# Optimization experiments

Hardware: AMD Instinct MI355X
Metric: run time of the kernel (lower is better)

## Reference

```python
import jax, jax.numpy as jnp
import numpy as np

B, H, S, D = 4, 16, 2048, 64  # head_dim = num_dims // num_heads = 1024 // 16


def setup_inputs() -> dict:
    key = jax.random.key(0)
    kq, kk, kv = jax.random.split(key, 3)
    q = jax.random.normal(kq, (B, H, S, D), dtype=jnp.float32)
    k = jax.random.normal(kk, (B, H, S, D), dtype=jnp.float32)
    v = jax.random.normal(kv, (B, H, S, D), dtype=jnp.float32)
    return {"q": q, "k": k, "v": v}


def reference(q, k, v):
    # scores = (q @ k^T) / sqrt(head_dim)  -> [B, H, S, S]
    scale = 1.0 / np.sqrt(D).astype(np.float32)
    scores = jnp.einsum("bhqd,bhkd->bhqk", q, k) * scale
    # softmax over keys; dropout rate is 0.0 (eval), so it's the identity
    weights = jax.nn.softmax(scores, axis=-1)
    # weights @ v -> [B, H, S, D]
    return jnp.einsum("bhqk,bhkd->bhqd", weights, v)
```

## Files before the change

### kernel.cpp

```cpp
#include <hip/hip_runtime.h>
#include <hip/hip_bf16.h>

#define S_LEN 2048
#define BH_TOTAL 64
#define D_DIM 64
#define NT 32

typedef float f32x4 __attribute__((ext_vector_type(4)));
typedef __bf16 bf16x8 __attribute__((ext_vector_type(8)));
typedef unsigned short u16x8 __attribute__((ext_vector_type(8)));
typedef unsigned int u32;
typedef u32 u32x2 __attribute__((ext_vector_type(2)));

union BF8 { u16x8 u; bf16x8 b; };

#if __has_builtin(__builtin_amdgcn_exp2f)
#define EX2(x) __builtin_amdgcn_exp2f(x)
#else
#define EX2(x) exp2f(x)
#endif

__device__ __forceinline__ unsigned short f2b(float f) {
  __bf16 h = (__bf16)f;
  return __builtin_bit_cast(unsigned short, h);
}
__device__ __forceinline__ u32 pk2(float a, float b) {
  return (u32)f2b(a) | ((u32)f2b(b) << 16);
}

__device__ __forceinline__ void gload16(const unsigned short* g, unsigned short* l) {
  __builtin_amdgcn_global_load_lds(
      (const __attribute__((address_space(1))) unsigned int*)g,
      (__attribute__((address_space(3))) unsigned int*)l, 16, 0, 0);
}

__global__ __launch_bounds__(256)
void cvt_k(const float* __restrict__ K, unsigned short* __restrict__ Kb) {
  int i = blockIdx.x * 256 + threadIdx.x;
  const f32x4* src = (const f32x4*)K;
  f32x4 a = src[2 * i], b = src[2 * i + 1];
  u16x8 o;
  #pragma unroll
  for (int j = 0; j < 4; ++j) { o[j] = f2b(a[j]); o[j + 4] = f2b(b[j]); }
  ((u16x8*)Kb)[i] = o;
}

__global__ __launch_bounds__(256)
void tr_v(const float* __restrict__ V, unsigned short* __restrict__ Vt) {
  __shared__ unsigned short T[64][72];
  int bh = blockIdx.x >> 5, t5 = blockIdx.x & 31;
  int s0 = t5 * 64;
  int tid = threadIdx.x;
  {
    int s = tid >> 2, d0 = (tid & 3) * 16;
    const float* src = V + ((size_t)bh * S_LEN + s0 + s) * D_DIM + d0;
    #pragma unroll
    for (int j = 0; j < 16; j += 4) {
      f32x4 x = *(const f32x4*)(src + j);
      #pragma unroll
      for (int q2 = 0; q2 < 4; ++q2) T[d0 + j + q2][s] = f2b(x[q2]);
    }
  }
  __syncthreads();
  {
    int d = tid >> 2, c0 = (tid & 3) * 16;
    unsigned short* dst = Vt + ((size_t)bh * D_DIM + d) * S_LEN + s0 + c0;
    u16x8 o;
    #pragma unroll
    for (int q2 = 0; q2 < 8; ++q2) o[q2] = T[d][c0 + q2];
    *(u16x8*)dst = o;
    #pragma unroll
    for (int q2 = 0; q2 < 8; ++q2) o[q2] = T[d][c0 + 8 + q2];
    *(u16x8*)(dst + 8) = o;
  }
}

__global__ __launch_bounds__(512, 4)
void attn_fwd(const float* __restrict__ Q, const unsigned short* __restrict__ Kb,
              const unsigned short* __restrict__ Vt, float* __restrict__ O) {
  const int wg = blockIdx.x;
  const int id = (wg & 7) * 64 + (wg >> 3);
  const int qt = id & 7;
  const int bh = id >> 3;

  const int tid = threadIdx.x;
  const int w = tid >> 6;
  const int ln = tid & 63;
  const int lr = ln & 15;
  const int lg = ln >> 4;

  __shared__ __align__(16) unsigned short Ks[2][4096];
  __shared__ __align__(16) unsigned short Vs[2][4096];
  __shared__ __align__(16) unsigned short Ps[8][2048];

  const size_t hbase = (size_t)bh * S_LEN * D_DIM;
  const unsigned short* Kh = Kb + hbase;
  const unsigned short* Vh = Vt + hbase;

  const int q0 = qt * 256 + w * 32;
  BF8 qf[2][2];
  {
    const float sc = 0.125f * 1.44269504088896f;
    #pragma unroll
    for (int qg = 0; qg < 2; ++qg) {
      const float* qp = Q + hbase + (size_t)(q0 + qg * 16 + lr) * D_DIM + lg * 8;
      #pragma unroll
      for (int f = 0; f < 2; ++f) {
        f32x4 a = *(const f32x4*)(qp + f * 32);
        f32x4 b = *(const f32x4*)(qp + f * 32 + 4);
        #pragma unroll
        for (int j = 0; j < 4; ++j) {
          qf[qg][f].u[j]     = f2b(a[j] * sc);
          qf[qg][f].u[j + 4] = f2b(b[j] * sc);
        }
      }
    }
  }

  const int srow = ln >> 3;
  const int scol = ((ln & 7) ^ srow) * 8;
  const unsigned short* ks0 = Kh + (size_t)(w * 8 + srow) * D_DIM + scol;
  const unsigned short* vs0 = Vh + (size_t)(w * 8 + srow) * S_LEN + scol;

  const int swz = (lr & 7) << 4;
  const int fo0 = lr * 128 + ((lg * 16) ^ swz);
  const int fo1 = fo0 ^ 64;
  const int pw0 = lr * 128 + ((lg * 8) ^ swz);

  f32x4 oacc[2][4];
  f32x4 lacc[2];
  #pragma unroll
  for (int qg = 0; qg < 2; ++qg) {
    #pragma unroll
    for (int j = 0; j < 4; ++j) lacc[qg][j] = 0.f;
    #pragma unroll
    for (int dt = 0; dt < 4; ++dt)
      #pragma unroll
      for (int j = 0; j < 4; ++j) oacc[qg][dt][j] = 0.f;
  }
  BF8 ones;
  #pragma unroll
  for (int j = 0; j < 8; ++j) ones.u[j] = 0x3F80;

  gload16(ks0, &Ks[0][w * 512]);
  gload16(vs0, &Vs[0][w * 512]);
  __syncthreads();

  for (int t = 0; t < NT; ++t) {
    const int cur = t & 1;
    if (t + 1 < NT) {
      gload16(ks0 + (size_t)(t + 1) * 4096, &Ks[cur ^ 1][w * 512]);
      gload16(vs0 + (size_t)(t + 1) * 64,   &Vs[cur ^ 1][w * 512]);
    }

    const char* KsB = (const char*)&Ks[cur][0];
    f32x4 s0[4], s1[4];
    #pragma unroll
    for (int ct = 0; ct < 4; ++ct)
      #pragma unroll
      for (int j = 0; j < 4; ++j) { s0[ct][j] = 0.f; s1[ct][j] = 0.f; }
    __builtin_amdgcn_s_setprio(1);
    #pragma unroll
    for (int f = 0; f < 2; ++f) {
      const int fo = f ? fo1 : fo0;
      #pragma unroll
      for (int ct = 0; ct < 4; ++ct) {
        BF8 kb; kb.u = *(const u16x8*)(KsB + fo + ct * 2048);
        s0[ct] = __builtin_amdgcn_mfma_f32_16x16x32_bf16(kb.b, qf[0][f].b, s0[ct], 0, 0, 0);
        s1[ct] = __builtin_amdgcn_mfma_f32_16x16x32_bf16(kb.b, qf[1][f].b, s1[ct], 0, 0, 0);
      }
    }
    __builtin_amdgcn_s_setprio(0);

    char* psb = (char*)&Ps[w][0];
    #pragma unroll
    for (int ct = 0; ct < 4; ++ct) {
      u32x2 pw;
      pw[0] = pk2(EX2(s0[ct][0]), EX2(s0[ct][1]));
      pw[1] = pk2(EX2(s0[ct][2]), EX2(s0[ct][3]));
      *(u32x2*)(psb + (pw0 ^ (ct * 32))) = pw;
    }
    #pragma unroll
    for (int ct = 0; ct < 4; ++ct) {
      u32x2 pw;
      pw[0] = pk2(EX2(s1[ct][0]), EX2(s1[ct][1]));
      pw[1] = pk2(EX2(s1[ct][2]), EX2(s1[ct][3]));
      *(u32x2*)(psb + 2048 + (pw0 ^ (ct * 32))) = pw;
    }

    const char* VsB = (const char*)&Vs[cur][0];
    __builtin_amdgcn_s_setprio(1);
    #pragma unroll
    for (int f = 0; f < 2; ++f) {
      const int fo = f ? fo1 : fo0;
      BF8 pa0, pa1;
      pa0.u = *(const u16x8*)(psb + fo);
      pa1.u = *(const u16x8*)(psb + 2048 + fo);
      lacc[0] = __builtin_amdgcn_mfma_f32_16x16x32_bf16(ones.b, pa0.b, lacc[0], 0, 0, 0);
      lacc[1] = __builtin_amdgcn_mfma_f32_16x16x32_bf16(ones.b, pa1.b, lacc[1], 0, 0, 0);
      #pragma unroll
      for (int dt = 0; dt < 4; ++dt) {
        BF8 vb; vb.u = *(const u16x8*)(VsB + fo + dt * 2048);
        oacc[0][dt] = __builtin_amdgcn_mfma_f32_16x16x32_bf16(vb.b, pa0.b, oacc[0][dt], 0, 0, 0);
        oacc[1][dt] = __builtin_amdgcn_mfma_f32_16x16x32_bf16(vb.b, pa1.b, oacc[1][dt], 0, 0, 0);
      }
    }
    __builtin_amdgcn_s_setprio(0);
    __syncthreads();
  }

  #pragma unroll
  for (int qg = 0; qg < 2; ++qg) {
    float inv = 1.0f / lacc[qg][0];
    float* op = O + hbase + (size_t)(q0 + qg * 16 + lr) * D_DIM;
    #pragma unroll
    for (int dt = 0; dt < 4; ++dt)
      #pragma unroll
      for (int r = 0; r < 4; ++r)
        op[dt * 16 + lg * 4 + r] = oacc[qg][dt][r] * inv;
  }
}

extern "C" void kernel_launch(void* const* d_in, const int* in_sizes, int n_in,
                              void* d_out, int out_size, void* d_ws, size_t ws_size,
                              hipStream_t stream) {
  const float* q = (const float*)d_in[0];
  const float* k = (const float*)d_in[1];
  const float* v = (const float*)d_in[2];
  float* o = (float*)d_out;
  unsigned short* kb = (unsigned short*)d_ws;
  unsigned short* vt = kb + (size_t)BH_TOTAL * S_LEN * D_DIM;

  cvt_k<<<dim3(4096), 256, 0, stream>>>(k, kb);
  tr_v<<<dim3(2048), 256, 0, stream>>>(v, vt);
  attn_fwd<<<dim3(512), 512, 0, stream>>>(q, kb, vt, o);
}
```

Measured before the change: 103.2 us.

## Switch attention to 32x32x16 MFMA with register-resident P via permlane swap

Rewrites the attention kernel to use 32x32x16 bf16 MFMAs. The exponentiated scores are rearranged in registers with permlane32 swaps instead of round-tripping through shared memory, which removes the P LDS buffer. The row sum is now accumulated with scalar adds instead of an extra MFMA against a ones vector. Blocks shrink to 256 threads with 1024 workgroups, which adds more redundant K/V tile loads per head and risks higher register pressure from the 16-wide accumulators.

```diff
diff --git a/kernel.cpp b/kernel.cpp
--- a/kernel.cpp
+++ b/kernel.cpp
@@ -7,12 +7,14 @@
 #define NT 32
 
 typedef float f32x4 __attribute__((ext_vector_type(4)));
+typedef float f32x16 __attribute__((ext_vector_type(16)));
 typedef __bf16 bf16x8 __attribute__((ext_vector_type(8)));
 typedef unsigned short u16x8 __attribute__((ext_vector_type(8)));
 typedef unsigned int u32;
 typedef u32 u32x2 __attribute__((ext_vector_type(2)));
-
-union BF8 { u16x8 u; bf16x8 b; };
+typedef u32 u32x4 __attribute__((ext_vector_type(4)));
+
+union BF8 { u32x4 w; u16x8 u; bf16x8 b; };
 
 #if __has_builtin(__builtin_amdgcn_exp2f)
 #define EX2(x) __builtin_amdgcn_exp2f(x)
@@ -26,6 +28,20 @@
 }
 __device__ __forceinline__ u32 pk2(float a, float b) {
   return (u32)f2b(a) | ((u32)f2b(b) << 16);
+}
+
+__device__ __forceinline__ u32x2 pl32(u32 x, u32 y) {
+#if __has_builtin(__builtin_amdgcn_permlane32_swap)
+  return __builtin_amdgcn_permlane32_swap(x, y, false, false);
+#else
+  u32 xs = (u32)__shfl_xor((int)x, 32);
+  u32 ys = (u32)__shfl_xor((int)y, 32);
+  int hi = (int)(threadIdx.x & 32);
+  u32x2 r;
+  r.x = hi ? ys : x;
+  r.y = hi ? y : xs;
+  return r;
+#endif
 }
 
 __device__ __forceinline__ void gload16(const unsigned short* g, unsigned short* l) {
@@ -75,149 +91,144 @@
   }
 }
 
-__global__ __launch_bounds__(512, 4)
+__global__ __launch_bounds__(256, 4)
 void attn_fwd(const float* __restrict__ Q, const unsigned short* __restrict__ Kb,
               const unsigned short* __restrict__ Vt, float* __restrict__ O) {
   const int wg = blockIdx.x;
-  const int id = (wg & 7) * 64 + (wg >> 3);
-  const int qt = id & 7;
-  const int bh = id >> 3;
+  const int id = (wg & 7) * 128 + (wg >> 3);
+  const int qt = id & 15;
+  const int bh = id >> 4;
 
   const int tid = threadIdx.x;
   const int w = tid >> 6;
   const int ln = tid & 63;
-  const int lr = ln & 15;
-  const int lg = ln >> 4;
+  const int l31 = ln & 31;
+  const int h = ln >> 5;
 
   __shared__ __align__(16) unsigned short Ks[2][4096];
   __shared__ __align__(16) unsigned short Vs[2][4096];
-  __shared__ __align__(16) unsigned short Ps[8][2048];
 
   const size_t hbase = (size_t)bh * S_LEN * D_DIM;
   const unsigned short* Kh = Kb + hbase;
   const unsigned short* Vh = Vt + hbase;
 
-  const int q0 = qt * 256 + w * 32;
-  BF8 qf[2][2];
+  const int q0 = qt * 128 + w * 32;
+
+  BF8 qf[4];
   {
     const float sc = 0.125f * 1.44269504088896f;
-    #pragma unroll
-    for (int qg = 0; qg < 2; ++qg) {
-      const float* qp = Q + hbase + (size_t)(q0 + qg * 16 + lr) * D_DIM + lg * 8;
-      #pragma unroll
-      for (int f = 0; f < 2; ++f) {
-        f32x4 a = *(const f32x4*)(qp + f * 32);
-        f32x4 b = *(const f32x4*)(qp + f * 32 + 4);
-        #pragma unroll
-        for (int j = 0; j < 4; ++j) {
-          qf[qg][f].u[j]     = f2b(a[j] * sc);
-          qf[qg][f].u[j + 4] = f2b(b[j] * sc);
-        }
+    const float* qp = Q + hbase + (size_t)(q0 + l31) * D_DIM + h * 8;
+    #pragma unroll
+    for (int f = 0; f < 4; ++f) {
+      f32x4 a = *(const f32x4*)(qp + f * 16);
+      f32x4 b = *(const f32x4*)(qp + f * 16 + 4);
+      #pragma unroll
+      for (int j = 0; j < 4; ++j) {
+        qf[f].u[j]     = f2b(a[j] * sc);
+        qf[f].u[j + 4] = f2b(b[j] * sc);
       }
     }
   }
 
   const int srow = ln >> 3;
   const int scol = ((ln & 7) ^ srow) * 8;
-  const unsigned short* ks0 = Kh + (size_t)(w * 8 + srow) * D_DIM + scol;
-  const unsigned short* vs0 = Vh + (size_t)(w * 8 + srow) * S_LEN + scol;
-
-  const int swz = (lr & 7) << 4;
-  const int fo0 = lr * 128 + ((lg * 16) ^ swz);
-  const int fo1 = fo0 ^ 64;
-  const int pw0 = lr * 128 + ((lg * 8) ^ swz);
-
-  f32x4 oacc[2][4];
-  f32x4 lacc[2];
+  const unsigned short* ks0 = Kh + (size_t)(w * 16 + srow) * D_DIM + scol;
+  const unsigned short* vs0 = Vh + (size_t)(w * 16 + srow) * S_LEN + scol;
+
+  const int swz = (ln & 7) << 4;
+  const int rb = l31 * 128;
+  int cx[4];
   #pragma unroll
-  for (int qg = 0; qg < 2; ++qg) {
-    #pragma unroll
-    for (int j = 0; j < 4; ++j) lacc[qg][j] = 0.f;
-    #pragma unroll
-    for (int dt = 0; dt < 4; ++dt)
-      #pragma unroll
-      for (int j = 0; j < 4; ++j) oacc[qg][dt][j] = 0.f;
-  }
-  BF8 ones;
+  for (int m = 0; m < 4; ++m) cx[m] = (m * 32 + h * 16) ^ swz;
+
+  f32x16 oa0, oa1;
   #pragma unroll
-  for (int j = 0; j < 8; ++j) ones.u[j] = 0x3F80;
-
-  gload16(ks0, &Ks[0][w * 512]);
-  gload16(vs0, &Vs[0][w * 512]);
+  for (int j = 0; j < 16; ++j) { oa0[j] = 0.f; oa1[j] = 0.f; }
+  float ls = 0.f;
+
+  gload16(ks0,            &Ks[0][w * 1024]);
+  gload16(ks0 + 512,      &Ks[0][w * 1024 + 512]);
+  gload16(vs0,            &Vs[0][w * 1024]);
+  gload16(vs0 + 8 * S_LEN, &Vs[0][w * 1024 + 512]);
   __syncthreads();
 
   for (int t = 0; t < NT; ++t) {
     const int cur = t & 1;
     if (t + 1 < NT) {
-      gload16(ks0 + (size_t)(t + 1) * 4096, &Ks[cur ^ 1][w * 512]);
-      gload16(vs0 + (size_t)(t + 1) * 64,   &Vs[cur ^ 1][w * 512]);
+      const unsigned short* kp = ks0 + (size_t)(t + 1) * 4096;
+      const unsigned short* vp = vs0 + (t + 1) * 64;
+      gload16(kp,             &Ks[cur ^ 1][w * 1024]);
+      gload16(kp + 512,       &Ks[cur ^ 1][w * 1024 + 512]);
+      gload16(vp,             &Vs[cur ^ 1][w * 1024]);
+      gload16(vp + 8 * S_LEN, &Vs[cur ^ 1][w * 1024 + 512]);
     }
 
     const char* KsB = (const char*)&Ks[cur][0];
-    f32x4 s0[4], s1[4];
-    #pragma unroll
-    for (int ct = 0; ct < 4; ++ct)
-      #pragma unroll
-      for (int j = 0; j < 4; ++j) { s0[ct][j] = 0.f; s1[ct][j] = 0.f; }
+    const char* VsB = (const char*)&Vs[cur][0];
+
+    f32x16 s0, s1;
+    #pragma unroll
+    for (int j = 0; j < 16; ++j) { s0[j] = 0.f; s1[j] = 0.f; }
     __builtin_amdgcn_s_setprio(1);
     #pragma unroll
-    for (int f = 0; f < 2; ++f) {
-      const int fo = f ? fo1 : fo0;
-      #pragma unroll
-      for (int ct = 0; ct < 4; ++ct) {
-        BF8 kb; kb.u = *(const u16x8*)(KsB + fo + ct * 2048);
-        s0[ct] = __builtin_amdgcn_mfma_f32_16x16x32_bf16(kb.b, qf[0][f].b, s0[ct], 0, 0, 0);
-        s1[ct] = __builtin_amdgcn_mfma_f32_16x16x32_bf16(kb.b, qf[1][f].b, s1[ct], 0, 0, 0);
-      }
+    for (int f = 0; f < 4; ++f) {
+      BF8 k0, k1;
+      k0.u = *(const u16x8*)(KsB + rb + cx[f]);
+      k1.u = *(const u16x8*)(KsB + 4096 + rb + cx[f]);
+      s0 = __builtin_amdgcn_mfma_f32_32x32x16_bf16(k0.b, qf[f].b, s0, 0, 0, 0);
+      s1 = __builtin_amdgcn_mfma_f32_32x32x16_bf16(k1.b, qf[f].b, s1, 0, 0, 0);
     }
     __builtin_amdgcn_s_setprio(0);
 
-    char* psb = (char*)&Ps[w][0];
-    #pragma unroll
-    for (int ct = 0; ct < 4; ++ct) {
-      u32x2 pw;
-      pw[0] = pk2(EX2(s0[ct][0]), EX2(s0[ct][1]));
-      pw[1] = pk2(EX2(s0[ct][2]), EX2(s0[ct][3]));
-      *(u32x2*)(psb + (pw0 ^ (ct * 32))) = pw;
-    }
-    #pragma unroll
-    for (int ct = 0; ct < 4; ++ct) {
-      u32x2 pw;
-      pw[0] = pk2(EX2(s1[ct][0]), EX2(s1[ct][1]));
-      pw[1] = pk2(EX2(s1[ct][2]), EX2(s1[ct][3]));
-      *(u32x2*)(psb + 2048 + (pw0 ^ (ct * 32))) = pw;
-    }
-
-    const char* VsB = (const char*)&Vs[cur][0];
-    __builtin_amdgcn_s_setprio(1);
-    #pragma unroll
-    for (int f = 0; f < 2; ++f) {
-      const int fo = f ? fo1 : fo0;
-      BF8 pa0, pa1;
-      pa0.u = *(const u16x8*)(psb + fo);
-      pa1.u = *(const u16x8*)(psb + 2048 + fo);
-      lacc[0] = __builtin_amdgcn_mfma_f32_16x16x32_bf16(ones.b, pa0.b, lacc[0], 0, 0, 0);
-      lacc[1] = __builtin_amdgcn_mfma_f32_16x16x32_bf16(ones.b, pa1.b, lacc[1], 0, 0, 0);
-      #pragma unroll
-      for (int dt = 0; dt < 4; ++dt) {
-        BF8 vb; vb.u = *(const u16x8*)(VsB + fo + dt * 2048);
-        oacc[0][dt] = __builtin_amdgcn_mfma_f32_16x16x32_bf16(vb.b, pa0.b, oacc[0][dt], 0, 0, 0);
-        oacc[1][dt] = __builtin_amdgcn_mfma_f32_16x16x32_bf16(vb.b, pa1.b, oacc[1][dt], 0, 0, 0);
-      }
-    }
-    __builtin_amdgcn_s_setprio(0);
+    #pragma unroll
+    for (int kt = 0; kt < 2; ++kt) {
+      const f32x16 sv = kt ? s1 : s0;
+      float p[16];
+      #pragma unroll
+      for (int j = 0; j < 16; ++j) p[j] = EX2(sv[j]);
+      ls += (((p[0] + p[1]) + (p[2] + p[3])) + ((p[4] + p[5]) + (p[6] + p[7])))
+          + (((p[8] + p[9]) + (p[10] + p[11])) + ((p[12] + p[13]) + (p[14] + p[15])));
+      u32 wlo[4], whi[4];
+      #pragma unroll
+      for (int b2 = 0; b2 < 4; ++b2) {
+        wlo[b2] = pk2(p[4 * b2 + 0], p[4 * b2 + 1]);
+        whi[b2] = pk2(p[4 * b2 + 2], p[4 * b2 + 3]);
+      }
+      #pragma unroll
+      for (int s = 0; s < 2; ++s) {
+        u32x2 rlo = pl32(wlo[2 * s], wlo[2 * s + 1]);
+        u32x2 rhi = pl32(whi[2 * s], whi[2 * s + 1]);
+        BF8 pf;
+        pf.w[0] = rlo.x; pf.w[1] = rhi.x; pf.w[2] = rlo.y; pf.w[3] = rhi.y;
+        BF8 v0, v1;
+        v0.u = *(const u16x8*)(VsB + rb + cx[kt * 2 + s]);
+        v1.u = *(const u16x8*)(VsB + 4096 + rb + cx[kt * 2 + s]);
+        __builtin_amdgcn_s_setprio(1);
+        oa0 = __builtin_amdgcn_mfma_f32_32x32x16_bf16(v0.b, pf.b, oa0, 0, 0, 0);
+        oa1 = __builtin_amdgcn_mfma_f32_32x32x16_bf16(v1.b, pf.b, oa1, 0, 0, 0);
+        __builtin_amdgcn_s_setprio(0);
+      }
+    }
     __syncthreads();
   }
 
-  #pragma unroll
-  for (int qg = 0; qg < 2; ++qg) {
-    float inv = 1.0f / lacc[qg][0];
-    float* op = O + hbase + (size_t)(q0 + qg * 16 + lr) * D_DIM;
-    #pragma unroll
-    for (int dt = 0; dt < 4; ++dt)
-      #pragma unroll
-      for (int r = 0; r < 4; ++r)
-        op[dt * 16 + lg * 4 + r] = oacc[qg][dt][r] * inv;
+  {
+    float lo2 = __shfl_xor(ls, 32);
+    float inv = 1.0f / (ls + lo2);
+    float* op = O + hbase + (size_t)(q0 + l31) * D_DIM;
+    #pragma unroll
+    for (int dt = 0; dt < 2; ++dt) {
+      const f32x16 oa = dt ? oa1 : oa0;
+      #pragma unroll
+      for (int b2 = 0; b2 < 4; ++b2) {
+        f32x4 vv;
+        vv[0] = oa[4 * b2 + 0] * inv;
+        vv[1] = oa[4 * b2 + 1] * inv;
+        vv[2] = oa[4 * b2 + 2] * inv;
+        vv[3] = oa[4 * b2 + 3] * inv;
+        *(f32x4*)(op + dt * 32 + b2 * 8 + h * 4) = vv;
+      }
+    }
   }
 }
 
@@ -233,5 +244,5 @@
 
   cvt_k<<<dim3(4096), 256, 0, stream>>>(k, kb);
   tr_v<<<dim3(2048), 256, 0, stream>>>(v, vt);
-  attn_fwd<<<dim3(512), 512, 0, stream>>>(q, kb, vt, o);
-}
+  attn_fwd<<<dim3(1024), 256, 0, stream>>>(q, kb, vt, o);
+}
```

Result: slower. 109.9 us (+6.5%).
